# Performance work log

Hardware: AMD Instinct MI355X
Metric: run time of the kernel (lower is better)

Reference implementation:

```python
import jax, jax.numpy as jnp
import numpy as np

THRESHOLD = 0.1      # threshold_pos; threshold_neg = -THRESHOLD (encode uses +THRESHOLD on -diff)
TIME_STEPS = 16
BETA = 4.0           # surrogate_beta for fast_sigmoid
REFRACTORY = 2       # refractory_period
EPS = 1e-8

@jax.custom_vjp
def spike_fn(v):
    # forward: hard threshold spike (0/1)
    return (v >= THRESHOLD).astype(jnp.float32)

def _spike_fwd(v):
    return spike_fn(v), v

def _spike_bwd(v, g):
    # fast-sigmoid surrogate gradient centered at threshold
    s = jax.nn.sigmoid(BETA * (v - THRESHOLD))
    return (g * BETA * s * (1.0 - s),)

spike_fn.defvjp(_spike_fwd, _spike_bwd)

def setup_inputs() -> dict:
    key = jax.random.key(0)
    cpc_features = jax.random.normal(key, (8, 4096, 128), dtype=jnp.float32)
    return {"cpc_features": cpc_features}

def reference(cpc_features):
    # cpc_features: [B, S, F] -- temporal-contrast encode each feature channel along S
    diff = jnp.diff(cpc_features, axis=1, prepend=cpc_features[:, :1, :])   # [B,S,F]
    std = jnp.std(diff, axis=1, keepdims=True)                              # [B,1,F]
    nd = diff / (std + EPS)
    pos = spike_fn(nd)      # positive-contrast spikes, [B,S,F]
    neg = spike_fn(-nd)     # negative-contrast spikes, [B,S,F]
    # refractory pattern over time steps: t%3==0 -> pos, t%3==1 -> neg, else silent
    phase = (jnp.arange(TIME_STEPS) % (REFRACTORY + 1))[None, :, None, None]  # [1,T,1,1]
    spikes = jnp.where(phase == 0, pos[:, None, :, :],
                       jnp.where(phase == 1, neg[:, None, :, :], 0.0))
    return spikes  # [B, T, S, F]
```

## Files before the change

### kernel.cpp

```cpp
#include <hip/hip_runtime.h>
#include <math.h>

typedef float f32x4 __attribute__((ext_vector_type(4)));

constexpr int kB = 8;
constexpr int kS = 4096;
constexpr int kF = 128;
constexpr int kT = 16;
constexpr int kNCHUNK = 64;
constexpr int kSCHUNK = kS / kNCHUNK;

__global__ __launch_bounds__(128) void std_partial_kernel(
    const float* __restrict__ x, double* __restrict__ psum, double* __restrict__ psq) {
    const int b = blockIdx.x / kNCHUNK;
    const int c = blockIdx.x % kNCHUNK;
    const int f = threadIdx.x;
    const long base = ((long)(b * kS + c * kSCHUNK)) * kF + f;
    float prev = (c == 0) ? x[(long)b * kS * kF + f] : x[base - kF];
    double s1 = 0.0, s2 = 0.0;
    #pragma unroll 4
    for (int j = 0; j < kSCHUNK; ++j) {
        float cur = x[base + (long)j * kF];
        float d = cur - prev;
        s1 += (double)d;
        s2 += (double)d * (double)d;
        prev = cur;
    }
    const int o = c * (kB * kF) + b * kF + f;
    psum[o] = s1;
    psq[o]  = s2;
}

__global__ __launch_bounds__(256) void std_finish_kernel(
    const double* __restrict__ psum, const double* __restrict__ psq,
    float* __restrict__ denom) {
    const int i = blockIdx.x * blockDim.x + threadIdx.x;
    if (i >= kB * kF) return;
    double s1 = 0.0, s2 = 0.0;
    #pragma unroll 8
    for (int c = 0; c < kNCHUNK; ++c) {
        s1 += psum[c * (kB * kF) + i];
        s2 += psq[c * (kB * kF) + i];
    }
    const double mean = s1 / (double)kS;
    double var = s2 / (double)kS - mean * mean;
    if (var < 0.0) var = 0.0;
    const float stdf = (float)sqrt(var);
    denom[i] = stdf + 1e-8f;
}

__global__ __launch_bounds__(128) void std_direct_kernel(
    const float* __restrict__ x, float* __restrict__ denom) {
    const int b = blockIdx.x;
    const int f = threadIdx.x;
    const long base = (long)b * kS * kF + f;
    float prev = x[base];
    double s1 = 0.0, s2 = 0.0;
    for (int s = 0; s < kS; ++s) {
        float cur = x[base + (long)s * kF];
        float d = cur - prev;
        s1 += (double)d;
        s2 += (double)d * (double)d;
        prev = cur;
    }
    const double mean = s1 / (double)kS;
    double var = s2 / (double)kS - mean * mean;
    if (var < 0.0) var = 0.0;
    denom[b * kF + f] = (float)sqrt(var) + 1e-8f;
}

__global__ __launch_bounds__(256) void spike_write_kernel(
    const float* __restrict__ x, const float* __restrict__ denom,
    float* __restrict__ out) {
    const int tid = threadIdx.x;
    const int f4 = tid & 31;
    const int sl = tid >> 5;
    const int b  = blockIdx.x >> 9;
    const int sc = blockIdx.x & 511;
    const int s  = sc * 8 + sl;

    const long inoff = ((long)(b * kS + s)) * kF + f4 * 4;
    const f32x4 cur  = *(const f32x4*)(x + inoff);
    const f32x4 prev = (s == 0) ? cur : *(const f32x4*)(x + inoff - kF);
    const f32x4 dn   = *(const f32x4*)(denom + b * kF + f4 * 4);

    f32x4 pos, neg;
    #pragma unroll
    for (int k = 0; k < 4; ++k) {
        const float d  = cur[k] - prev[k];
        const float nd = d / dn[k];
        pos[k] = (nd  >= 0.1f) ? 1.0f : 0.0f;
        neg[k] = (-nd >= 0.1f) ? 1.0f : 0.0f;
    }
    f32x4 zero;
    zero[0] = 0.0f; zero[1] = 0.0f; zero[2] = 0.0f; zero[3] = 0.0f;

    const long slice = (long)kS * kF;
    const long outbase = (((long)b * kT) * kS + s) * kF + f4 * 4;
    #pragma unroll
    for (int t = 0; t < kT; ++t) {
        const int ph = t % 3;
        const f32x4 v = (ph == 0) ? pos : ((ph == 1) ? neg : zero);
        __builtin_nontemporal_store(v, (f32x4*)(out + outbase + (long)t * slice));
    }
}

extern "C" void kernel_launch(void* const* d_in, const int* in_sizes, int n_in,
                              void* d_out, int out_size, void* d_ws, size_t ws_size,
                              hipStream_t stream) {
    const float* x = (const float*)d_in[0];
    float* out = (float*)d_out;

    float* denom = (float*)d_ws;
    double* psum = (double*)((char*)d_ws + 4096);
    double* psq  = psum + (size_t)kNCHUNK * kB * kF;
    const size_t needed = 4096 + 2ull * kNCHUNK * kB * kF * sizeof(double);

    if (ws_size >= needed) {
        std_partial_kernel<<<kB * kNCHUNK, 128, 0, stream>>>(x, psum, psq);
        std_finish_kernel<<<(kB * kF + 255) / 256, 256, 0, stream>>>(psum, psq, denom);
    } else {
        std_direct_kernel<<<kB, 128, 0, stream>>>(x, denom);
    }
    spike_write_kernel<<<kB * (kS / 8), 256, 0, stream>>>(x, denom, out);
}
```

Baseline: 290.6 us.

## Stage spikes in shared memory for contiguous output writes; split std into more chunks

The spike writer now handles 32 rows per block. It stages the pos/neg spikes in LDS, then writes each time-step slice as a contiguous 16KB span using regular stores instead of nontemporal ones. The std partial kernel splits the sequence into four times as many chunks and preloads each chunk's values into registers so the loads can overlap. The intent is more parallelism in the reduction and better-shaped bulk writes, at the cost of a barrier, extra LDS traffic, and losing the nontemporal hint on a write-bound kernel.

Result: no change. 296.4 us (+2.0%).

```diff
diff --git a/kernel.cpp b/kernel.cpp
--- a/kernel.cpp
+++ b/kernel.cpp
@@ -7,8 +7,9 @@
 constexpr int kS = 4096;
 constexpr int kF = 128;
 constexpr int kT = 16;
-constexpr int kNCHUNK = 64;
+constexpr int kNCHUNK = 256;
 constexpr int kSCHUNK = kS / kNCHUNK;
+constexpr int kRows = 32;
 
 __global__ __launch_bounds__(128) void std_partial_kernel(
     const float* __restrict__ x, double* __restrict__ psum, double* __restrict__ psq) {
@@ -17,14 +18,16 @@
     const int f = threadIdx.x;
     const long base = ((long)(b * kS + c * kSCHUNK)) * kF + f;
     float prev = (c == 0) ? x[(long)b * kS * kF + f] : x[base - kF];
+    float cur[kSCHUNK];
+    #pragma unroll
+    for (int j = 0; j < kSCHUNK; ++j) cur[j] = x[base + (long)j * kF];
     double s1 = 0.0, s2 = 0.0;
-    #pragma unroll 4
+    #pragma unroll
     for (int j = 0; j < kSCHUNK; ++j) {
-        float cur = x[base + (long)j * kF];
-        float d = cur - prev;
+        float d = cur[j] - prev;
         s1 += (double)d;
         s2 += (double)d * (double)d;
-        prev = cur;
+        prev = cur[j];
     }
     const int o = c * (kB * kF) + b * kF + f;
     psum[o] = s1;
@@ -37,7 +40,6 @@
     const int i = blockIdx.x * blockDim.x + threadIdx.x;
     if (i >= kB * kF) return;
     double s1 = 0.0, s2 = 0.0;
-    #pragma unroll 8
     for (int c = 0; c < kNCHUNK; ++c) {
         s1 += psum[c * (kB * kF) + i];
         s2 += psq[c * (kB * kF) + i];
@@ -72,36 +74,55 @@
 __global__ __launch_bounds__(256) void spike_write_kernel(
     const float* __restrict__ x, const float* __restrict__ denom,
     float* __restrict__ out) {
+    __shared__ float pos_s[kRows * kF];
+    __shared__ float neg_s[kRows * kF];
     const int tid = threadIdx.x;
     const int f4 = tid & 31;
     const int sl = tid >> 5;
-    const int b  = blockIdx.x >> 9;
-    const int sc = blockIdx.x & 511;
-    const int s  = sc * 8 + sl;
+    const int b  = blockIdx.x >> 7;
+    const int sc = blockIdx.x & 127;
+    const int s0 = sc * kRows;
 
-    const long inoff = ((long)(b * kS + s)) * kF + f4 * 4;
-    const f32x4 cur  = *(const f32x4*)(x + inoff);
-    const f32x4 prev = (s == 0) ? cur : *(const f32x4*)(x + inoff - kF);
-    const f32x4 dn   = *(const f32x4*)(denom + b * kF + f4 * 4);
+    const f32x4 dn = *(const f32x4*)(denom + b * kF + f4 * 4);
 
-    f32x4 pos, neg;
     #pragma unroll
-    for (int k = 0; k < 4; ++k) {
-        const float d  = cur[k] - prev[k];
-        const float nd = d / dn[k];
-        pos[k] = (nd  >= 0.1f) ? 1.0f : 0.0f;
-        neg[k] = (-nd >= 0.1f) ? 1.0f : 0.0f;
+    for (int r = sl; r < kRows; r += 8) {
+        const int s = s0 + r;
+        const long off = ((long)(b * kS + s)) * kF + f4 * 4;
+        const f32x4 cur  = *(const f32x4*)(x + off);
+        const f32x4 prev = (s == 0) ? cur : *(const f32x4*)(x + off - kF);
+        f32x4 p, n;
+        #pragma unroll
+        for (int k = 0; k < 4; ++k) {
+            const float nd = (cur[k] - prev[k]) / dn[k];
+            p[k] = (nd  >= 0.1f) ? 1.0f : 0.0f;
+            n[k] = (-nd >= 0.1f) ? 1.0f : 0.0f;
+        }
+        *(f32x4*)(pos_s + r * kF + f4 * 4) = p;
+        *(f32x4*)(neg_s + r * kF + f4 * 4) = n;
     }
+    __syncthreads();
+
     f32x4 zero;
     zero[0] = 0.0f; zero[1] = 0.0f; zero[2] = 0.0f; zero[3] = 0.0f;
 
     const long slice = (long)kS * kF;
-    const long outbase = (((long)b * kT) * kS + s) * kF + f4 * 4;
-    #pragma unroll
+    const long outb = (((long)b * kT) * kS + s0) * kF;
     for (int t = 0; t < kT; ++t) {
         const int ph = t % 3;
-        const f32x4 v = (ph == 0) ? pos : ((ph == 1) ? neg : zero);
-        __builtin_nontemporal_store(v, (f32x4*)(out + outbase + (long)t * slice));
+        float* dst = out + outb + (long)t * slice;
+        if (ph == 2) {
+            #pragma unroll
+            for (int i = 0; i < 4; ++i)
+                *(f32x4*)(dst + (i * 256 + tid) * 4) = zero;
+        } else {
+            const float* src = (ph == 0) ? pos_s : neg_s;
+            #pragma unroll
+            for (int i = 0; i < 4; ++i) {
+                const f32x4 v = *(const f32x4*)(src + (i * 256 + tid) * 4);
+                *(f32x4*)(dst + (i * 256 + tid) * 4) = v;
+            }
+        }
     }
 }
 
@@ -122,5 +143,5 @@
     } else {
         std_direct_kernel<<<kB, 128, 0, stream>>>(x, denom);
     }
-    spike_write_kernel<<<kB * (kS / 8), 256, 0, stream>>>(x, denom, out);
+    spike_write_kernel<<<kB * (kS / kRows), 256, 0, stream>>>(x, denom, out);
 }
```
